# Optimization experiments

Hardware: AMD Instinct MI355X
Metric: run time of the kernel (lower is better)

Reference implementation:

```python
import jax, jax.numpy as jnp
import numpy as np

N = 100000   # nodes
E = 1600000  # edges
NF, EF = 128, 16      # node_features, edge_features
NFIL, EFIL = 64, 32   # node_filters, edge_filters
C = 16                # classes


def setup_inputs() -> dict:
    key = jax.random.key(0)
    ks = jax.random.split(key, 12)
    s = 0.1
    return {
        "x": jax.random.normal(ks[0], (N, NF), jnp.float32),
        "edge_index": jax.random.randint(ks[1], (2, E), 0, N),
        "edge_x": jax.random.normal(ks[2], (E, EF), jnp.float32),
        # edge MLP params
        "W1": jax.random.normal(ks[3], (EF, EFIL), jnp.float32) * s,
        "b1": jnp.zeros((EFIL,), jnp.float32),
        "W2": jax.random.normal(ks[4], (EFIL, 1), jnp.float32) * s,
        "b2": jnp.zeros((1,), jnp.float32),
        # GCN layer params
        "Wc1": jax.random.normal(ks[5], (NF, NFIL), jnp.float32) * s,
        "bc1": jnp.zeros((NFIL,), jnp.float32),
        "Wc2": jax.random.normal(ks[6], (NFIL, C), jnp.float32) * s,
        "bc2": jnp.zeros((C,), jnp.float32),
    }


def gcn_conv(x, src, tgt, w, W, b, n):
    # PyG GCNConv with edge_weight: x @ W, symmetric norm, scatter-add, + bias.
    x = x @ W                                             # [n, out]
    deg = jax.ops.segment_sum(w, tgt, num_segments=n)     # weighted degree incl. self-loops
    dinv = jnp.where(deg > 0, jax.lax.rsqrt(deg), 0.0)
    norm = dinv[src] * w * dinv[tgt]                      # [E+n]
    out = jax.ops.segment_sum(norm[:, None] * x[src], tgt, num_segments=n)
    return out + b


def reference(x, edge_index, edge_x, W1, b1, W2, b2, Wc1, bc1, Wc2, bc2):
    # edge MLP -> scalar attention weight per edge
    h = jax.nn.relu(edge_x @ W1 + b1)
    ew = jax.nn.sigmoid(h @ W2 + b2).reshape(-1)          # [E]
    src, tgt = edge_index[0], edge_index[1]
    # add self-loops with weight 1 (as GCNConv does internally)
    loop = jnp.arange(N)
    src_f = jnp.concatenate([src, loop])
    tgt_f = jnp.concatenate([tgt, loop])
    ew_f = jnp.concatenate([ew, jnp.ones((N,), ew.dtype)])
    h1 = jax.nn.relu(gcn_conv(x, src_f, tgt_f, ew_f, Wc1, bc1, N))
    # dropout omitted: eval mode (F.dropout is identity when training=False)
    h2 = gcn_conv(h1, src_f, tgt_f, ew_f, Wc2, bc2, N)
    return jax.nn.log_softmax(h2, axis=1)
```

## Files before the change

### kernel.cpp

```cpp
#include <hip/hip_runtime.h>
#include <math.h>

#define NFD 128
#define EF_ 16
#define EFIL 32
#define NFIL 64
#define CLS 16

typedef unsigned int uint;
typedef unsigned long long ull;
typedef unsigned short ushort;

__device__ inline void fma4(float4& a, float s, const float4& w) {
  a.x = fmaf(s, w.x, a.x); a.y = fmaf(s, w.y, a.y);
  a.z = fmaf(s, w.z, a.z); a.w = fmaf(s, w.w, a.w);
}

__device__ inline uint bf16_rn(float f) {
  uint u = __float_as_uint(f);
  return (u + 0x7FFFu + ((u >> 16) & 1u)) >> 16;
}
__device__ inline float entw(uint lo) {
  return __uint_as_float((lo >> 17) << 16);
}

__global__ __launch_bounds__(256) void edge_mlp_link_kernel(
    const float* __restrict__ edge_x, const int* __restrict__ ei,
    const float* __restrict__ W1, const float* __restrict__ b1,
    const float* __restrict__ W2, const float* __restrict__ b2,
    int* __restrict__ head, ull* __restrict__ nextbuf, int E) {
  __shared__ __align__(16) float sW1[EF_ * EFIL];
  __shared__ float sb1[EFIL];
  __shared__ float sW2[EFIL];
  __shared__ float sb2v;
  int t = threadIdx.x;
  for (int idx = t; idx < EF_ * EFIL / 4; idx += 256)
    reinterpret_cast<float4*>(sW1)[idx] = reinterpret_cast<const float4*>(W1)[idx];
  if (t < EFIL) { sb1[t] = b1[t]; sW2[t] = W2[t]; }
  if (t == 64) sb2v = b2[0];
  __syncthreads();
  int e = blockIdx.x * 256 + t;
  if (e >= E) return;
  int sv = ei[e], tg = ei[(size_t)E + e];
  int old = atomicExch(&head[(size_t)tg * 8 + (blockIdx.x & 7)], e);
  const float4* ex4 = reinterpret_cast<const float4*>(edge_x) + (size_t)e * (EF_ / 4);
  float ex[EF_];
  #pragma unroll
  for (int q = 0; q < EF_ / 4; q++) {
    float4 v = ex4[q];
    ex[4*q+0] = v.x; ex[4*q+1] = v.y; ex[4*q+2] = v.z; ex[4*q+3] = v.w;
  }
  float acc[EFIL];
  #pragma unroll
  for (int j = 0; j < EFIL; j++) acc[j] = sb1[j];
  #pragma unroll
  for (int k = 0; k < EF_; k++) {
    float xk = ex[k];
    #pragma unroll
    for (int j4 = 0; j4 < EFIL / 4; j4++) {
      float4 w = reinterpret_cast<const float4*>(sW1)[k * (EFIL/4) + j4];
      acc[4*j4+0] = fmaf(xk, w.x, acc[4*j4+0]);
      acc[4*j4+1] = fmaf(xk, w.y, acc[4*j4+1]);
      acc[4*j4+2] = fmaf(xk, w.z, acc[4*j4+2]);
      acc[4*j4+3] = fmaf(xk, w.w, acc[4*j4+3]);
    }
  }
  float s = sb2v;
  #pragma unroll
  for (int j = 0; j < EFIL; j++) s = fmaf(fmaxf(acc[j], 0.f), sW2[j], s);
  float sig = 1.0f / (1.0f + __expf(-s));
  uint lo = ((bf16_rn(sig) & 0x7FFFu) << 17) | (uint)sv;
  nextbuf[e] = ((ull)(uint)old << 32) | lo;
}

__global__ __launch_bounds__(256) void walk_kernel(
    const int* __restrict__ head, const ull* __restrict__ nextbuf,
    uint* __restrict__ slotc, int* __restrict__ grp_cnt,
    float* __restrict__ dinv, int caprows, int n) {
  int i = blockIdx.x * blockDim.x + threadIdx.x;
  if (i >= n) return;
  int4 ha = *reinterpret_cast<const int4*>(head + (size_t)i * 8);
  int4 hb = *reinterpret_cast<const int4*>(head + (size_t)i * 8 + 4);
  int ev0 = ha.x, ev1 = ha.y, ev2 = ha.z, ev3 = ha.w;
  int ev4 = hb.x, ev5 = hb.y, ev6 = hb.z, ev7 = hb.w;
  int cnt = 0;
  float sum = 0.f;
  bool any = (ev0 | ev1 | ev2 | ev3 | ev4 | ev5 | ev6 | ev7) != -1 ||
             (ev0 >= 0 || ev1 >= 0 || ev2 >= 0 || ev3 >= 0 ||
              ev4 >= 0 || ev5 >= 0 || ev6 >= 0 || ev7 >= 0);
  while (any) {
    ull v0 = 0, v1 = 0, v2 = 0, v3 = 0, v4 = 0, v5 = 0, v6 = 0, v7 = 0;
    if (ev0 >= 0) v0 = nextbuf[ev0];
    if (ev1 >= 0) v1 = nextbuf[ev1];
    if (ev2 >= 0) v2 = nextbuf[ev2];
    if (ev3 >= 0) v3 = nextbuf[ev3];
    if (ev4 >= 0) v4 = nextbuf[ev4];
    if (ev5 >= 0) v5 = nextbuf[ev5];
    if (ev6 >= 0) v6 = nextbuf[ev6];
    if (ev7 >= 0) v7 = nextbuf[ev7];
    #define STEP(EV, VV)                                              \
    if (EV >= 0) {                                                    \
      uint lo = (uint)VV; sum += entw(lo);                            \
      if (cnt < caprows) slotc[(size_t)cnt * n + i] = lo;             \
      cnt++; EV = (int)(uint)(VV >> 32);                              \
    }
    STEP(ev0, v0) STEP(ev1, v1) STEP(ev2, v2) STEP(ev3, v3)
    STEP(ev4, v4) STEP(ev5, v5) STEP(ev6, v6) STEP(ev7, v7)
    #undef STEP
    any = ev0 >= 0 || ev1 >= 0 || ev2 >= 0 || ev3 >= 0 ||
          ev4 >= 0 || ev5 >= 0 || ev6 >= 0 || ev7 >= 0;
  }
  grp_cnt[i] = min(cnt, caprows);
  dinv[i] = rsqrtf(1.0f + sum);
}

__global__ __launch_bounds__(256) void gemm1_kernel(
    const float* __restrict__ x, const float* __restrict__ Wc1,
    uint* __restrict__ xwb, int n) {
  __shared__ __align__(16) float sW[NFD * NFIL];
  int t = threadIdx.x;
  for (int idx = t; idx < NFD * NFIL / 4; idx += 256)
    reinterpret_cast<float4*>(sW)[idx] = reinterpret_cast<const float4*>(Wc1)[idx];
  __syncthreads();
  int tc = t & 15;
  int tr = t >> 4;
  int nrb = (n + 31) >> 5;
  const float4* sW4 = reinterpret_cast<const float4*>(sW);
  for (int rb = blockIdx.x; rb < nrb; rb += gridDim.x) {
    int r0 = rb * 32 + tr * 2;
    int r1 = r0 + 1;
    int c0 = r0 < n ? r0 : n - 1;
    int c1 = r1 < n ? r1 : n - 1;
    const float4* xr0 = reinterpret_cast<const float4*>(x + (size_t)c0 * NFD);
    const float4* xr1 = reinterpret_cast<const float4*>(x + (size_t)c1 * NFD);
    float4 a0 = {0, 0, 0, 0}, a1 = {0, 0, 0, 0};
    #pragma unroll 4
    for (int k4 = 0; k4 < NFD / 4; k4++) {
      float4 xa = xr0[k4];
      float4 xb = xr1[k4];
      float4 w0 = sW4[(k4*4+0)*16 + tc];
      float4 w1 = sW4[(k4*4+1)*16 + tc];
      float4 w2 = sW4[(k4*4+2)*16 + tc];
      float4 w3 = sW4[(k4*4+3)*16 + tc];
      fma4(a0, xa.x, w0); fma4(a0, xa.y, w1); fma4(a0, xa.z, w2); fma4(a0, xa.w, w3);
      fma4(a1, xb.x, w0); fma4(a1, xb.y, w1); fma4(a1, xb.z, w2); fma4(a1, xb.w, w3);
    }
    if (r0 < n) {
      uint2 o = {bf16_rn(a0.x) | (bf16_rn(a0.y) << 16),
                 bf16_rn(a0.z) | (bf16_rn(a0.w) << 16)};
      reinterpret_cast<uint2*>(xwb + (size_t)r0 * 32)[tc] = o;
    }
    if (r1 < n) {
      uint2 o = {bf16_rn(a1.x) | (bf16_rn(a1.y) << 16),
                 bf16_rn(a1.z) | (bf16_rn(a1.w) << 16)};
      reinterpret_cast<uint2*>(xwb + (size_t)r1 * 32)[tc] = o;
    }
  }
}

__global__ __launch_bounds__(256) void agg1_fused_kernel(
    const int* __restrict__ grp_cnt, const uint* __restrict__ slotc,
    const float* __restrict__ dinv, const uint* __restrict__ xwb,
    const float* __restrict__ bc1, const float* __restrict__ Wc2,
    ushort* __restrict__ ywb, int n) {
  __shared__ float sh[16][NFIL + 4];
  __shared__ float sW2[NFIL * CLS];
  __shared__ float sb1[NFIL];
  int t = threadIdx.x;
  for (int i = t; i < NFIL * CLS; i += 256) sW2[i] = Wc2[i];
  if (t < NFIL) sb1[t] = bc1[t];
  __syncthreads();
  int r = t >> 4;
  int node = blockIdx.x * 16 + r;
  int f4 = t & 15;
  bool ok = node < n;
  int nd = ok ? node : 0;
  int cnt = ok ? grp_cnt[nd] : 0;
  const uint2* xw2 = reinterpret_cast<const uint2*>(xwb);
  float d = ok ? dinv[nd] : 0.f;
  uint2 g = xw2[(size_t)nd * 16 + f4];
  float4 acc = {d * __uint_as_float(g.x << 16),
                d * __uint_as_float(g.x & 0xFFFF0000u),
                d * __uint_as_float(g.y << 16),
                d * __uint_as_float(g.y & 0xFFFF0000u)};
  int p = 0;
  for (; p + 1 < cnt; p += 2) {
    uint v0 = slotc[(size_t)p * n + nd];
    uint v1 = slotc[(size_t)(p + 1) * n + nd];
    int s0 = v0 & 0x1FFFF, s1 = v1 & 0x1FFFF;
    float w0 = entw(v0) * dinv[s0];
    float w1 = entw(v1) * dinv[s1];
    uint2 g0 = xw2[(size_t)s0 * 16 + f4];
    uint2 g1 = xw2[(size_t)s1 * 16 + f4];
    acc.x = fmaf(w0, __uint_as_float(g0.x << 16), acc.x);
    acc.y = fmaf(w0, __uint_as_float(g0.x & 0xFFFF0000u), acc.y);
    acc.z = fmaf(w0, __uint_as_float(g0.y << 16), acc.z);
    acc.w = fmaf(w0, __uint_as_float(g0.y & 0xFFFF0000u), acc.w);
    acc.x = fmaf(w1, __uint_as_float(g1.x << 16), acc.x);
    acc.y = fmaf(w1, __uint_as_float(g1.x & 0xFFFF0000u), acc.y);
    acc.z = fmaf(w1, __uint_as_float(g1.y << 16), acc.z);
    acc.w = fmaf(w1, __uint_as_float(g1.y & 0xFFFF0000u), acc.w);
  }
  if (p < cnt) {
    uint v0 = slotc[(size_t)p * n + nd];
    int s0 = v0 & 0x1FFFF;
    float w0 = entw(v0) * dinv[s0];
    uint2 g0 = xw2[(size_t)s0 * 16 + f4];
    acc.x = fmaf(w0, __uint_as_float(g0.x << 16), acc.x);
    acc.y = fmaf(w0, __uint_as_float(g0.x & 0xFFFF0000u), acc.y);
    acc.z = fmaf(w0, __uint_as_float(g0.y << 16), acc.z);
    acc.w = fmaf(w0, __uint_as_float(g0.y & 0xFFFF0000u), acc.w);
  }
  sh[r][4*f4 + 0] = fmaxf(fmaf(d, acc.x, sb1[4*f4 + 0]), 0.f);
  sh[r][4*f4 + 1] = fmaxf(fmaf(d, acc.y, sb1[4*f4 + 1]), 0.f);
  sh[r][4*f4 + 2] = fmaxf(fmaf(d, acc.z, sb1[4*f4 + 2]), 0.f);
  sh[r][4*f4 + 3] = fmaxf(fmaf(d, acc.w, sb1[4*f4 + 3]), 0.f);
  __syncthreads();
  {
    int j = t & 15;
    float o = 0.f;
    #pragma unroll
    for (int k = 0; k < NFIL; k++) o = fmaf(sh[r][k], sW2[k * CLS + j], o);
    if (ok) ywb[(size_t)node * CLS + j] = (ushort)bf16_rn(o);
  }
}

__global__ __launch_bounds__(256) void agg2_fused_kernel(
    const int* __restrict__ grp_cnt, const uint* __restrict__ slotc,
    const float* __restrict__ dinv, const ushort* __restrict__ ywb,
    const float* __restrict__ bc2, float* __restrict__ out, int n) {
  __shared__ float sb2[CLS];
  int t = threadIdx.x;
  if (t < CLS) sb2[t] = bc2[t];
  __syncthreads();
  int node = blockIdx.x * 16 + (t >> 4);
  int j = t & 15;
  bool ok = node < n;
  int nd = ok ? node : 0;
  int cnt = ok ? grp_cnt[nd] : 0;
  float d = ok ? dinv[nd] : 0.f;
  float acc = d * __uint_as_float((uint)ywb[(size_t)nd * CLS + j] << 16);
  int p = 0;
  for (; p + 1 < cnt; p += 2) {
    uint v0 = slotc[(size_t)p * n + nd];
    uint v1 = slotc[(size_t)(p + 1) * n + nd];
    int s0 = v0 & 0x1FFFF, s1 = v1 & 0x1FFFF;
    float w0 = entw(v0) * dinv[s0];
    float w1 = entw(v1) * dinv[s1];
    float y0 = __uint_as_float((uint)ywb[(size_t)s0 * CLS + j] << 16);
    float y1 = __uint_as_float((uint)ywb[(size_t)s1 * CLS + j] << 16);
    acc = fmaf(w0, y0, acc);
    acc = fmaf(w1, y1, acc);
  }
  if (p < cnt) {
    uint v0 = slotc[(size_t)p * n + nd];
    int s0 = v0 & 0x1FFFF;
    float w0 = entw(v0) * dinv[s0];
    acc = fmaf(w0, __uint_as_float((uint)ywb[(size_t)s0 * CLS + j] << 16), acc);
  }
  float v = fmaf(d, acc, sb2[j]);
  float m = v;
  m = fmaxf(m, __shfl_xor(m, 1, 16));
  m = fmaxf(m, __shfl_xor(m, 2, 16));
  m = fmaxf(m, __shfl_xor(m, 4, 16));
  m = fmaxf(m, __shfl_xor(m, 8, 16));
  float ex = __expf(v - m);
  float ssum = ex;
  ssum += __shfl_xor(ssum, 1, 16);
  ssum += __shfl_xor(ssum, 2, 16);
  ssum += __shfl_xor(ssum, 4, 16);
  ssum += __shfl_xor(ssum, 8, 16);
  if (ok) out[(size_t)node * CLS + j] = (v - m) - __logf(ssum);
}

extern "C" void kernel_launch(void* const* d_in, const int* in_sizes, int n_in,
                              void* d_out, int out_size, void* d_ws, size_t ws_size,
                              hipStream_t stream) {
  const float* x      = (const float*)d_in[0];
  const int*   ei     = (const int*)d_in[1];
  const float* edge_x = (const float*)d_in[2];
  const float* W1     = (const float*)d_in[3];
  const float* b1     = (const float*)d_in[4];
  const float* W2     = (const float*)d_in[5];
  const float* b2     = (const float*)d_in[6];
  const float* Wc1    = (const float*)d_in[7];
  const float* bc1    = (const float*)d_in[8];
  const float* Wc2    = (const float*)d_in[9];
  const float* bc2    = (const float*)d_in[10];
  float* outp = (float*)d_out;
  int n = in_sizes[0] / NFD;
  int E = in_sizes[1] / 2;

  int cap = 48;
  while (cap > 32 && 8.0 * E + (double)n * (200.0 + 4.0 * cap) > (double)ws_size)
    cap -= 8;

  char* base = (char*)d_ws;
  int* head = (int*)base;            base += (size_t)n * 32;
  ull* nextbuf = (ull*)base;         base += (size_t)E * 8;
  uint* slotc = (uint*)base;         base += (size_t)n * cap * 4;
  int* grp_cnt = (int*)base;         base += (size_t)n * 4;
  float* dinv = (float*)base;        base += (size_t)n * 4;
  uint* xwb = (uint*)base;           base += (size_t)n * 128;
  ushort* ywb = (ushort*)base;

  int nblk16 = (n + 15) / 16;
  int nblk256 = (n + 255) / 256;
  hipMemsetAsync(head, 0xFF, (size_t)n * 32, stream);
  edge_mlp_link_kernel<<<(E + 255) / 256, 256, 0, stream>>>(
      edge_x, ei, W1, b1, W2, b2, head, nextbuf, E);
  walk_kernel<<<nblk256, 256, 0, stream>>>(head, nextbuf, slotc, grp_cnt, dinv, cap, n);
  gemm1_kernel<<<1024, 256, 0, stream>>>(x, Wc1, xwb, n);
  agg1_fused_kernel<<<nblk16, 256, 0, stream>>>(grp_cnt, slotc, dinv, xwb, bc1, Wc2, ywb, n);
  agg2_fused_kernel<<<nblk16, 256, 0, stream>>>(grp_cnt, slotc, dinv, ywb, bc2, outp, n);
}
```

Measured before the change: 230.5 us.

## Merge node GEMM into edge MLP launch and prescale layer-2 features by dinv

Moves the x@Wc1 GEMM into the edge-MLP kernel: every 7th block runs GEMM row tiles and the other blocks handle edges, so both independent stages share one launch and overlap. Layer-1 aggregation stores y already multiplied by the node's dinv, so layer-2 aggregation no longer gathers dinv[src] for every edge. Both gather loops are also unrolled to four edges per iteration. The cost is a 32 KB dynamic shared allocation for every block, including edge blocks that need far less, which can lower occupancy for the edge work. The 1:6 block split is a fixed heuristic.

```diff
diff --git a/kernel.cpp b/kernel.cpp
--- a/kernel.cpp
+++ b/kernel.cpp
@@ -24,25 +24,75 @@
   return __uint_as_float((lo >> 17) << 16);
 }
 
-__global__ __launch_bounds__(256) void edge_mlp_link_kernel(
+__global__ __launch_bounds__(256) void edge_gemm_kernel(
     const float* __restrict__ edge_x, const int* __restrict__ ei,
     const float* __restrict__ W1, const float* __restrict__ b1,
     const float* __restrict__ W2, const float* __restrict__ b2,
-    int* __restrict__ head, ull* __restrict__ nextbuf, int E) {
-  __shared__ __align__(16) float sW1[EF_ * EFIL];
-  __shared__ float sb1[EFIL];
-  __shared__ float sW2[EFIL];
-  __shared__ float sb2v;
+    int* __restrict__ head, ull* __restrict__ nextbuf, int E,
+    const float* __restrict__ x, const float* __restrict__ Wc1,
+    uint* __restrict__ xwb, int n, int NBG) {
+  extern __shared__ __align__(16) char smem[];
   int t = threadIdx.x;
+  int bid = blockIdx.x;
+  int gq = (bid + 1) / 7;
+  bool is_gemm = ((bid + 1) % 7) == 0;
+
+  if (is_gemm) {
+    float* sW = (float*)smem;
+    for (int idx = t; idx < NFD * NFIL / 4; idx += 256)
+      reinterpret_cast<float4*>(sW)[idx] = reinterpret_cast<const float4*>(Wc1)[idx];
+    __syncthreads();
+    int tc = t & 15;
+    int tr = t >> 4;
+    int nrb = (n + 31) >> 5;
+    const float4* sW4 = reinterpret_cast<const float4*>(sW);
+    for (int rb = gq - 1; rb < nrb; rb += NBG) {
+      int r0 = rb * 32 + tr * 2;
+      int r1 = r0 + 1;
+      int c0 = r0 < n ? r0 : n - 1;
+      int c1 = r1 < n ? r1 : n - 1;
+      const float4* xr0 = reinterpret_cast<const float4*>(x + (size_t)c0 * NFD);
+      const float4* xr1 = reinterpret_cast<const float4*>(x + (size_t)c1 * NFD);
+      float4 a0 = {0, 0, 0, 0}, a1 = {0, 0, 0, 0};
+      #pragma unroll 4
+      for (int k4 = 0; k4 < NFD / 4; k4++) {
+        float4 xa = xr0[k4];
+        float4 xb = xr1[k4];
+        float4 w0 = sW4[(k4*4+0)*16 + tc];
+        float4 w1 = sW4[(k4*4+1)*16 + tc];
+        float4 w2 = sW4[(k4*4+2)*16 + tc];
+        float4 w3 = sW4[(k4*4+3)*16 + tc];
+        fma4(a0, xa.x, w0); fma4(a0, xa.y, w1); fma4(a0, xa.z, w2); fma4(a0, xa.w, w3);
+        fma4(a1, xb.x, w0); fma4(a1, xb.y, w1); fma4(a1, xb.z, w2); fma4(a1, xb.w, w3);
+      }
+      if (r0 < n) {
+        uint2 o = {bf16_rn(a0.x) | (bf16_rn(a0.y) << 16),
+                   bf16_rn(a0.z) | (bf16_rn(a0.w) << 16)};
+        reinterpret_cast<uint2*>(xwb + (size_t)r0 * 32)[tc] = o;
+      }
+      if (r1 < n) {
+        uint2 o = {bf16_rn(a1.x) | (bf16_rn(a1.y) << 16),
+                   bf16_rn(a1.z) | (bf16_rn(a1.w) << 16)};
+        reinterpret_cast<uint2*>(xwb + (size_t)r1 * 32)[tc] = o;
+      }
+    }
+    return;
+  }
+
+  int eidx = bid - gq;
+  float* sW1 = (float*)smem;
+  float* sb1 = sW1 + EF_ * EFIL;
+  float* sW2 = sb1 + EFIL;
+  float* sb2 = sW2 + EFIL;
   for (int idx = t; idx < EF_ * EFIL / 4; idx += 256)
     reinterpret_cast<float4*>(sW1)[idx] = reinterpret_cast<const float4*>(W1)[idx];
   if (t < EFIL) { sb1[t] = b1[t]; sW2[t] = W2[t]; }
-  if (t == 64) sb2v = b2[0];
+  if (t == 64) sb2[0] = b2[0];
   __syncthreads();
-  int e = blockIdx.x * 256 + t;
+  int e = eidx * 256 + t;
   if (e >= E) return;
   int sv = ei[e], tg = ei[(size_t)E + e];
-  int old = atomicExch(&head[(size_t)tg * 8 + (blockIdx.x & 7)], e);
+  int old = atomicExch(&head[(size_t)tg * 8 + (eidx & 7)], e);
   const float4* ex4 = reinterpret_cast<const float4*>(edge_x) + (size_t)e * (EF_ / 4);
   float ex[EF_];
   #pragma unroll
@@ -65,7 +115,7 @@
       acc[4*j4+3] = fmaf(xk, w.w, acc[4*j4+3]);
     }
   }
-  float s = sb2v;
+  float s = sb2[0];
   #pragma unroll
   for (int j = 0; j < EFIL; j++) s = fmaf(fmaxf(acc[j], 0.f), sW2[j], s);
   float sig = 1.0f / (1.0f + __expf(-s));
@@ -85,9 +135,8 @@
   int ev4 = hb.x, ev5 = hb.y, ev6 = hb.z, ev7 = hb.w;
   int cnt = 0;
   float sum = 0.f;
-  bool any = (ev0 | ev1 | ev2 | ev3 | ev4 | ev5 | ev6 | ev7) != -1 ||
-             (ev0 >= 0 || ev1 >= 0 || ev2 >= 0 || ev3 >= 0 ||
-              ev4 >= 0 || ev5 >= 0 || ev6 >= 0 || ev7 >= 0);
+  bool any = ev0 >= 0 || ev1 >= 0 || ev2 >= 0 || ev3 >= 0 ||
+             ev4 >= 0 || ev5 >= 0 || ev6 >= 0 || ev7 >= 0;
   while (any) {
     ull v0 = 0, v1 = 0, v2 = 0, v3 = 0, v4 = 0, v5 = 0, v6 = 0, v7 = 0;
     if (ev0 >= 0) v0 = nextbuf[ev0];
@@ -112,50 +161,6 @@
   }
   grp_cnt[i] = min(cnt, caprows);
   dinv[i] = rsqrtf(1.0f + sum);
-}
-
-__global__ __launch_bounds__(256) void gemm1_kernel(
-    const float* __restrict__ x, const float* __restrict__ Wc1,
-    uint* __restrict__ xwb, int n) {
-  __shared__ __align__(16) float sW[NFD * NFIL];
-  int t = threadIdx.x;
-  for (int idx = t; idx < NFD * NFIL / 4; idx += 256)
-    reinterpret_cast<float4*>(sW)[idx] = reinterpret_cast<const float4*>(Wc1)[idx];
-  __syncthreads();
-  int tc = t & 15;
-  int tr = t >> 4;
-  int nrb = (n + 31) >> 5;
-  const float4* sW4 = reinterpret_cast<const float4*>(sW);
-  for (int rb = blockIdx.x; rb < nrb; rb += gridDim.x) {
-    int r0 = rb * 32 + tr * 2;
-    int r1 = r0 + 1;
-    int c0 = r0 < n ? r0 : n - 1;
-    int c1 = r1 < n ? r1 : n - 1;
-    const float4* xr0 = reinterpret_cast<const float4*>(x + (size_t)c0 * NFD);
-    const float4* xr1 = reinterpret_cast<const float4*>(x + (size_t)c1 * NFD);
-    float4 a0 = {0, 0, 0, 0}, a1 = {0, 0, 0, 0};
-    #pragma unroll 4
-    for (int k4 = 0; k4 < NFD / 4; k4++) {
-      float4 xa = xr0[k4];
-      float4 xb = xr1[k4];
-      float4 w0 = sW4[(k4*4+0)*16 + tc];
-      float4 w1 = sW4[(k4*4+1)*16 + tc];
-      float4 w2 = sW4[(k4*4+2)*16 + tc];
-      float4 w3 = sW4[(k4*4+3)*16 + tc];
-      fma4(a0, xa.x, w0); fma4(a0, xa.y, w1); fma4(a0, xa.z, w2); fma4(a0, xa.w, w3);
-      fma4(a1, xb.x, w0); fma4(a1, xb.y, w1); fma4(a1, xb.z, w2); fma4(a1, xb.w, w3);
-    }
-    if (r0 < n) {
-      uint2 o = {bf16_rn(a0.x) | (bf16_rn(a0.y) << 16),
-                 bf16_rn(a0.z) | (bf16_rn(a0.w) << 16)};
-      reinterpret_cast<uint2*>(xwb + (size_t)r0 * 32)[tc] = o;
-    }
-    if (r1 < n) {
-      uint2 o = {bf16_rn(a1.x) | (bf16_rn(a1.y) << 16),
-                 bf16_rn(a1.z) | (bf16_rn(a1.w) << 16)};
-      reinterpret_cast<uint2*>(xwb + (size_t)r1 * 32)[tc] = o;
-    }
-  }
 }
 
 __global__ __launch_bounds__(256) void agg1_fused_kernel(
@@ -183,34 +188,29 @@
                 d * __uint_as_float(g.x & 0xFFFF0000u),
                 d * __uint_as_float(g.y << 16),
                 d * __uint_as_float(g.y & 0xFFFF0000u)};
+  #define A1STEP(VV)                                                  \
+  {                                                                   \
+    int s_ = VV & 0x1FFFF;                                            \
+    float w_ = entw(VV) * dinv[s_];                                   \
+    uint2 g_ = xw2[(size_t)s_ * 16 + f4];                             \
+    acc.x = fmaf(w_, __uint_as_float(g_.x << 16), acc.x);             \
+    acc.y = fmaf(w_, __uint_as_float(g_.x & 0xFFFF0000u), acc.y);     \
+    acc.z = fmaf(w_, __uint_as_float(g_.y << 16), acc.z);             \
+    acc.w = fmaf(w_, __uint_as_float(g_.y & 0xFFFF0000u), acc.w);     \
+  }
   int p = 0;
-  for (; p + 1 < cnt; p += 2) {
+  for (; p + 3 < cnt; p += 4) {
     uint v0 = slotc[(size_t)p * n + nd];
     uint v1 = slotc[(size_t)(p + 1) * n + nd];
-    int s0 = v0 & 0x1FFFF, s1 = v1 & 0x1FFFF;
-    float w0 = entw(v0) * dinv[s0];
-    float w1 = entw(v1) * dinv[s1];
-    uint2 g0 = xw2[(size_t)s0 * 16 + f4];
-    uint2 g1 = xw2[(size_t)s1 * 16 + f4];
-    acc.x = fmaf(w0, __uint_as_float(g0.x << 16), acc.x);
-    acc.y = fmaf(w0, __uint_as_float(g0.x & 0xFFFF0000u), acc.y);
-    acc.z = fmaf(w0, __uint_as_float(g0.y << 16), acc.z);
-    acc.w = fmaf(w0, __uint_as_float(g0.y & 0xFFFF0000u), acc.w);
-    acc.x = fmaf(w1, __uint_as_float(g1.x << 16), acc.x);
-    acc.y = fmaf(w1, __uint_as_float(g1.x & 0xFFFF0000u), acc.y);
-    acc.z = fmaf(w1, __uint_as_float(g1.y << 16), acc.z);
-    acc.w = fmaf(w1, __uint_as_float(g1.y & 0xFFFF0000u), acc.w);
-  }
-  if (p < cnt) {
+    uint v2 = slotc[(size_t)(p + 2) * n + nd];
+    uint v3 = slotc[(size_t)(p + 3) * n + nd];
+    A1STEP(v0) A1STEP(v1) A1STEP(v2) A1STEP(v3)
+  }
+  for (; p < cnt; p++) {
     uint v0 = slotc[(size_t)p * n + nd];
-    int s0 = v0 & 0x1FFFF;
-    float w0 = entw(v0) * dinv[s0];
-    uint2 g0 = xw2[(size_t)s0 * 16 + f4];
-    acc.x = fmaf(w0, __uint_as_float(g0.x << 16), acc.x);
-    acc.y = fmaf(w0, __uint_as_float(g0.x & 0xFFFF0000u), acc.y);
-    acc.z = fmaf(w0, __uint_as_float(g0.y << 16), acc.z);
-    acc.w = fmaf(w0, __uint_as_float(g0.y & 0xFFFF0000u), acc.w);
-  }
+    A1STEP(v0)
+  }
+  #undef A1STEP
   sh[r][4*f4 + 0] = fmaxf(fmaf(d, acc.x, sb1[4*f4 + 0]), 0.f);
   sh[r][4*f4 + 1] = fmaxf(fmaf(d, acc.y, sb1[4*f4 + 1]), 0.f);
   sh[r][4*f4 + 2] = fmaxf(fmaf(d, acc.z, sb1[4*f4 + 2]), 0.f);
@@ -221,7 +221,7 @@
     float o = 0.f;
     #pragma unroll
     for (int k = 0; k < NFIL; k++) o = fmaf(sh[r][k], sW2[k * CLS + j], o);
-    if (ok) ywb[(size_t)node * CLS + j] = (ushort)bf16_rn(o);
+    if (ok) ywb[(size_t)node * CLS + j] = (ushort)bf16_rn(d * o);
   }
 }
 
@@ -239,25 +239,27 @@
   int nd = ok ? node : 0;
   int cnt = ok ? grp_cnt[nd] : 0;
   float d = ok ? dinv[nd] : 0.f;
-  float acc = d * __uint_as_float((uint)ywb[(size_t)nd * CLS + j] << 16);
+  float acc = __uint_as_float((uint)ywb[(size_t)nd * CLS + j] << 16);
+  #define A2STEP(VV)                                                       \
+  {                                                                        \
+    int s_ = VV & 0x1FFFF;                                                 \
+    acc = fmaf(entw(VV),                                                   \
+               __uint_as_float((uint)ywb[(size_t)s_ * CLS + j] << 16),     \
+               acc);                                                       \
+  }
   int p = 0;
-  for (; p + 1 < cnt; p += 2) {
+  for (; p + 3 < cnt; p += 4) {
     uint v0 = slotc[(size_t)p * n + nd];
     uint v1 = slotc[(size_t)(p + 1) * n + nd];
-    int s0 = v0 & 0x1FFFF, s1 = v1 & 0x1FFFF;
-    float w0 = entw(v0) * dinv[s0];
-    float w1 = entw(v1) * dinv[s1];
-    float y0 = __uint_as_float((uint)ywb[(size_t)s0 * CLS + j] << 16);
-    float y1 = __uint_as_float((uint)ywb[(size_t)s1 * CLS + j] << 16);
-    acc = fmaf(w0, y0, acc);
-    acc = fmaf(w1, y1, acc);
-  }
-  if (p < cnt) {
+    uint v2 = slotc[(size_t)(p + 2) * n + nd];
+    uint v3 = slotc[(size_t)(p + 3) * n + nd];
+    A2STEP(v0) A2STEP(v1) A2STEP(v2) A2STEP(v3)
+  }
+  for (; p < cnt; p++) {
     uint v0 = slotc[(size_t)p * n + nd];
-    int s0 = v0 & 0x1FFFF;
-    float w0 = entw(v0) * dinv[s0];
-    acc = fmaf(w0, __uint_as_float((uint)ywb[(size_t)s0 * CLS + j] << 16), acc);
-  }
+    A2STEP(v0)
+  }
+  #undef A2STEP
   float v = fmaf(d, acc, sb2[j]);
   float m = v;
   m = fmaxf(m, __shfl_xor(m, 1, 16));
@@ -304,13 +306,18 @@
   uint* xwb = (uint*)base;           base += (size_t)n * 128;
   ushort* ywb = (ushort*)base;
 
+  int NBE = (E + 255) / 256;
+  int T = NBE;
+  for (int it = 0; it < 8; it++) T = NBE + T / 7;
+  while (T - T / 7 < NBE) T++;
+  int NBG = T / 7;
+
   int nblk16 = (n + 15) / 16;
   int nblk256 = (n + 255) / 256;
   hipMemsetAsync(head, 0xFF, (size_t)n * 32, stream);
-  edge_mlp_link_kernel<<<(E + 255) / 256, 256, 0, stream>>>(
-      edge_x, ei, W1, b1, W2, b2, head, nextbuf, E);
+  edge_gemm_kernel<<<T, 256, 32768, stream>>>(
+      edge_x, ei, W1, b1, W2, b2, head, nextbuf, E, x, Wc1, xwb, n, NBG);
   walk_kernel<<<nblk256, 256, 0, stream>>>(head, nextbuf, slotc, grp_cnt, dinv, cap, n);
-  gemm1_kernel<<<1024, 256, 0, stream>>>(x, Wc1, xwb, n);
   agg1_fused_kernel<<<nblk16, 256, 0, stream>>>(grp_cnt, slotc, dinv, xwb, bc1, Wc2, ywb, n);
   agg2_fused_kernel<<<nblk16, 256, 0, stream>>>(grp_cnt, slotc, dinv, ywb, bc2, outp, n);
 }
```

New measurement: 195.3 us. -15.3%, faster.
